# Kernel tuning notes

Measured on AMD Instinct MI355X. Metric: run time of the kernel, lower is better.

Reference implementation:

```python
import jax, jax.numpy as jnp
import numpy as np

LAMBD = 0.2   # model.lambd
T_MAX = 1000  # model.T
TOL = 1e-10


def _softshrink(v, lam):
    return jnp.sign(v) * jnp.maximum(jnp.abs(v) - lam, 0.0)


def setup_inputs() -> dict:
    key = jax.random.key(0)
    k1, k2, k3 = jax.random.split(key, 3)
    n, m, N = 64, 256, 1024
    D = jax.random.normal(k1, (n, m), dtype=jnp.float32)
    D = D / jnp.linalg.norm(D, axis=0)                      # unit-norm atoms
    w = jax.random.normal(k2, (m,), dtype=jnp.float32)
    w = w / jnp.linalg.norm(w)
    x = jax.random.normal(k3, (N, n), dtype=jnp.float32)
    x = x / jnp.linalg.norm(x, axis=1, keepdims=True)       # unit-norm samples (as in generate_data)
    return {"x": x, "D": D, "w": w}


def _encode(x_t, D, lambd):
    # x_t: (n, N), D: (n, m). Faithful to encode(): ISTA with detached D/x,
    # then per-sample least-squares refinement on the support (vectorized as
    # a masked batched solve instead of a python loop over samples).
    m = D.shape[1]
    Dg = jax.lax.stop_gradient(D)
    xg = jax.lax.stop_gradient(x_t)
    # eta = 1/||D||_2^2 is a constant in torch (computed from numpy at init)
    eta = jax.lax.stop_gradient(1.0 / jnp.linalg.norm(Dg, ord=2) ** 2)
    thr = lambd * eta

    z0 = _softshrink(eta * (Dg.T @ xg), thr)                # (m, N)

    def cond(c):
        i, _, diff = c
        return (i < T_MAX) & (diff >= TOL)

    def body(c):
        i, z, _ = c
        res = Dg @ z - xg                                   # (n, N)
        znew = _softshrink(z - eta * (Dg.T @ res), thr)     # (m, N)
        return (i + 1, znew, jnp.linalg.norm(znew - z))

    _, z, _ = jax.lax.while_loop(
        cond, body, (jnp.int32(0), z0, jnp.array(jnp.inf, dtype=x_t.dtype))
    )
    z = jax.lax.stop_gradient(z)                            # ISTA output is fully detached in torch

    # Support refinement: alfa[S,i] = inv(D_S^T D_S) (D_S^T x_i - lambd*signs_S)
    mask = z != 0                                           # (m, N) support sets
    signs = jnp.sign(z)                                     # constant (sign has zero grad)
    M = mask.T.astype(x_t.dtype)                            # (N, m)
    G = D.T @ D                                             # (m, m) Gram (with grad, model.D)
    b = M * (x_t.T @ D - lambd * signs.T)                   # (N, m), zero off-support
    # Masked Gram: identity on off-support rows/cols -> block solve equals submatrix solve
    A = M[:, :, None] * M[:, None, :] * G[None] \
        + jnp.eye(m, dtype=x_t.dtype) * (1.0 - M)[:, :, None]   # (N, m, m)
    solved = jnp.linalg.solve(A, b[..., None])[..., 0]      # (N, m)
    alfa = jnp.where(mask, solved.T, z)                     # (m, N)
    return alfa


def reference(x, D, w):
    # x: (N, n). forward(): z = encode(x); y = w @ z; pred = [y, -y]
    z = _encode(x.T, D, LAMBD)                              # (m, N)
    y = w @ z                                               # (N,)
    return jnp.stack([y, -y], axis=1)                       # (N, 2)
```

## Files before the change

### kernel.cpp

```cpp
#include <hip/hip_runtime.h>

#define LAMBD 0.2f
#define KMAX 128
#define KS 64

using half8 = __attribute__((ext_vector_type(8))) _Float16;
using f32x4 = __attribute__((ext_vector_type(4))) float;

__device__ __forceinline__ float sshrink(float v, float thr) {
    float c = fminf(fmaxf(v, -thr), thr);
    return v - c;
}

__device__ __forceinline__ unsigned pack2(_Float16 a, _Float16 b) {
    unsigned short ua = __builtin_bit_cast(unsigned short, a);
    unsigned short ub = __builtin_bit_cast(unsigned short, b);
    return (unsigned)ua | ((unsigned)ub << 16);
}

__global__ __launch_bounds__(256) void prep_all(const float* __restrict__ xg,
                                                const float* __restrict__ Dg,
                                                float* __restrict__ ws,
                                                float* __restrict__ Gfull,
                                                float* __restrict__ cbuf)
{
    const int t = threadIdx.x;
    if (blockIdx.x == 0) {
        __shared__ __align__(16) float Dc[256 * 68];
        __shared__ __align__(16) float Bm[64 * 68];
        __shared__ float vv[64];
        __shared__ float part[4 * 64];
        __shared__ float lamsh;

        for (int i = 0; i < 64; ++i)
            Dc[t * 68 + i] = Dg[i * 256 + t];
        __syncthreads();

        const int ti = t >> 4, tj = t & 15;
        float acc[4][4];
        #pragma unroll
        for (int r = 0; r < 4; ++r)
            #pragma unroll
            for (int c = 0; c < 4; ++c) acc[r][c] = 0.f;
        for (int mm = 0; mm < 256; ++mm) {
            const float4 A = *(const float4*)&Dc[mm * 68 + 4 * ti];
            const float4 Bv = *(const float4*)&Dc[mm * 68 + 4 * tj];
            const float Ae[4] = {A.x, A.y, A.z, A.w};
            const float Be[4] = {Bv.x, Bv.y, Bv.z, Bv.w};
            #pragma unroll
            for (int r = 0; r < 4; ++r)
                #pragma unroll
                for (int c = 0; c < 4; ++c)
                    acc[r][c] += Ae[r] * Be[c];
        }
        #pragma unroll
        for (int r = 0; r < 4; ++r)
            #pragma unroll
            for (int c = 0; c < 4; ++c)
                Bm[(4 * ti + r) * 68 + (4 * tj + c)] = acc[r][c];
        if (t < 64) vv[t] = 0.125f;
        __syncthreads();

        for (int itp = 0; itp < 40; ++itp) {
            const int p = t >> 6, i = t & 63;
            float partial = 0.f;
            #pragma unroll
            for (int jj = 0; jj < 16; ++jj) {
                const int j = p * 16 + jj;
                partial += Bm[j * 68 + i] * vv[j];
            }
            part[p * 64 + i] = partial;
            __syncthreads();
            if (t < 64) {
                float nv = part[t] + part[64 + t] + part[128 + t] + part[192 + t];
                float n2 = nv * nv;
                for (int d = 1; d < 64; d <<= 1) n2 += __shfl_xor(n2, d);
                vv[t] = nv * rsqrtf(n2);
                if (t == 0) lamsh = n2;
            }
            __syncthreads();
        }
        if (t == 0) ws[0] = 1.0f / sqrtf(lamsh);
    } else {
        __shared__ float xsh[4][64];
        const int r = blockIdx.x - 1;
        const int s0 = r * 4;
        xsh[t >> 6][t & 63] = xg[s0 * 64 + t];
        __syncthreads();

        float accG = 0.f, a0 = 0.f, a1 = 0.f, a2 = 0.f, a3 = 0.f;
        #pragma unroll
        for (int i = 0; i < 64; ++i) {
            const float dv = Dg[i * 256 + t];
            const float dr = Dg[i * 256 + r];
            accG += dr * dv;
            a0 += xsh[0][i] * dv;
            a1 += xsh[1][i] * dv;
            a2 += xsh[2][i] * dv;
            a3 += xsh[3][i] * dv;
        }
        Gfull[r * 256 + t] = accG;
        cbuf[(s0 + 0) * 256 + t] = a0;
        cbuf[(s0 + 1) * 256 + t] = a1;
        cbuf[(s0 + 2) * 256 + t] = a2;
        cbuf[(s0 + 3) * 256 + t] = a3;
    }
}

__global__ __launch_bounds__(256, 1) void ista_solve(const float* __restrict__ cbuf,
                                                     const float* __restrict__ Gfull,
                                                     const float* __restrict__ ws,
                                                     const float* __restrict__ wg,
                                                     float* __restrict__ out)
{
    __shared__ __align__(16) _Float16 dbuf[2][16][264];
    __shared__ int chgs[4];
    __shared__ __align__(16) float znb[4][264];
    __shared__ __align__(16) float GmPool[16640];
    __shared__ int   idxPool[256];
    __shared__ float sgnPool[256];
    __shared__ float rhsF[KMAX];
    __shared__ float solF[KMAX];
    __shared__ int   big4[4];
    __shared__ int   kbig;

    const int t = threadIdx.x;
    const int w = t >> 6, l = t & 63;
    const int n = l & 15, kg = l >> 4;
    const int s0 = blockIdx.x * 4;
    const float s = ws[0];
    const float thr = LAMBD * s;
    const float S = 1.0f / 2048.0f;
    const float FLUSH = 6.2e-5f;

    half8 wh[4][8], wl[4][8];
    #pragma unroll
    for (int a = 0; a < 4; ++a) {
        const int row = 64 * w + 16 * a + n;
        #pragma unroll
        for (int kt = 0; kt < 8; ++kt) {
            const float4 g0 = *(const float4*)&Gfull[row * 256 + kt * 32 + kg * 8];
            const float4 g1 = *(const float4*)&Gfull[row * 256 + kt * 32 + kg * 8 + 4];
            const float ge[8] = {g0.x, g0.y, g0.z, g0.w, g1.x, g1.y, g1.z, g1.w};
            half8 h, lo;
            #pragma unroll
            for (int j = 0; j < 8; ++j) {
                const int col = kt * 32 + kg * 8 + j;
                const float wv = (row == col ? 1.0f : 0.0f) - s * ge[j];
                const _Float16 whj = (_Float16)wv;
                h[j] = whj;
                lo[j] = (_Float16)((wv - (float)whj) * 2048.0f);
            }
            wh[a][kt] = h;
            wl[a][kt] = lo;
        }
    }

    float bv[4][4], y[4][4], zo[4][4], zn[4][4];
    #pragma unroll
    for (int a = 0; a < 4; ++a)
        #pragma unroll
        for (int jj = 0; jj < 4; ++jj) {
            const int row = 64 * w + 16 * a + 4 * kg + jj;
            bv[a][jj] = (n < 4) ? s * cbuf[(s0 + n) * 256 + row] : 0.f;
            y[a][jj] = 0.f;
            zo[a][jj] = 0.f;
        }

    f32x4 acc1[4], acc2[4];
    #pragma unroll
    for (int a = 0; a < 4; ++a) {
        acc1[a] = (f32x4){0.f, 0.f, 0.f, 0.f};
        acc2[a] = (f32x4){0.f, 0.f, 0.f, 0.f};
    }

    float tk = 1.0f;
    int cur = 0;
    for (int it = 0; ; ++it) {
        const float tk1 = 0.5f * (1.0f + sqrtf(1.0f + 4.0f * tk * tk));
        const float beta = (tk - 1.0f) / tk1;
        bool anyflag = false;
        _Float16 dh16[4][4];
        #pragma unroll
        for (int a = 0; a < 4; ++a)
            #pragma unroll
            for (int jj = 0; jj < 4; ++jj) {
                const float P = acc1[a][jj] + S * acc2[a][jj];
                const float z = sshrink(P + bv[a][jj], thr);
                zn[a][jj] = z;
                const float yn = z + beta * (z - zo[a][jj]);
                zo[a][jj] = z;
                const float d = yn - y[a][jj];
                const bool live = fabsf(d) >= FLUSH;
                anyflag |= live;
                const _Float16 hd = live ? (_Float16)d : (_Float16)0.0f;
                dh16[a][jj] = hd;
                y[a][jj] += (float)hd;
            }
        tk = tk1;
        if (it == 1000) break;

        const int anyw = __any(anyflag);
        if (l == 0) chgs[w] = anyw;
        #pragma unroll
        for (int a = 0; a < 4; ++a) {
            const unsigned lo = pack2(dh16[a][0], dh16[a][1]);
            const unsigned hi = pack2(dh16[a][2], dh16[a][3]);
            *(uint2*)&dbuf[cur][n][64 * w + 16 * a + 4 * kg] = make_uint2(lo, hi);
        }
        __syncthreads();
        if (!(chgs[0] | chgs[1] | chgs[2] | chgs[3])) break;

        half8 dh[8];
        #pragma unroll
        for (int kt = 0; kt < 8; ++kt)
            dh[kt] = *(const half8*)&dbuf[cur][n][kt * 32 + kg * 8];

        #pragma unroll
        for (int kt = 0; kt < 8; ++kt)
            #pragma unroll
            for (int a = 0; a < 4; ++a) {
                acc1[a] = __builtin_amdgcn_mfma_f32_16x16x32_f16(wh[a][kt], dh[kt], acc1[a], 0, 0, 0);
                acc2[a] = __builtin_amdgcn_mfma_f32_16x16x32_f16(wl[a][kt], dh[kt], acc2[a], 0, 0, 0);
            }
        cur ^= 1;
    }

    if (n < 4) {
        #pragma unroll
        for (int a = 0; a < 4; ++a) {
            float4 v = make_float4(zn[a][0], zn[a][1], zn[a][2], zn[a][3]);
            *(float4*)&znb[n][64 * w + 16 * a + 4 * kg] = v;
        }
    }
    __syncthreads();

    const int sample = s0 + w;
    float* Gw = GmPool + w * (KS * (KS + 1));
    int*   idxW = idxPool + w * KS;
    float* sgnW = sgnPool + w * KS;

    const float4 zz = *(const float4*)&znb[w][4 * l];
    const int c0 = zz.x != 0.f, c1 = zz.y != 0.f, c2 = zz.z != 0.f, c3 = zz.w != 0.f;
    const int cnt = c0 + c1 + c2 + c3;
    int scan = cnt;
    for (int d = 1; d < 64; d <<= 1) {
        const int v = __shfl_up(scan, d);
        if (l >= d) scan += v;
    }
    int o = scan - cnt;
    const int k = __shfl(scan, 63);
    if (l == 0) big4[w] = (k > KS) ? 1 : 0;

    if (k == 0) {
        if (l == 0) { out[sample * 2] = 0.f; out[sample * 2 + 1] = 0.f; }
    } else if (k <= KS) {
        if (c0) { idxW[o] = 4 * l + 0; sgnW[o] = zz.x > 0.f ? 1.f : -1.f; ++o; }
        if (c1) { idxW[o] = 4 * l + 1; sgnW[o] = zz.y > 0.f ? 1.f : -1.f; ++o; }
        if (c2) { idxW[o] = 4 * l + 2; sgnW[o] = zz.z > 0.f ? 1.f : -1.f; ++o; }
        if (c3) { idxW[o] = 4 * l + 3; sgnW[o] = zz.w > 0.f ? 1.f : -1.f; ++o; }
        __builtin_amdgcn_wave_barrier();

        const int   ib = idxW[(l < k) ? l : (k - 1)];
        const float sg = (l < k) ? sgnW[l] : 0.f;
        float rhs = (l < k) ? (cbuf[sample * 256 + ib] - LAMBD * sg) : 0.f;

        for (int a = 0; a < k; ++a) {
            const int ra = __shfl(ib, a);
            if (l < k) Gw[a * (KS + 1) + l] = Gfull[ra * 256 + ib];
        }
        __builtin_amdgcn_wave_barrier();

        float dinv = 0.f;
        for (int j = 0; j < k; ++j) {
            const float Gjj = Gw[j * (KS + 1) + j];
            const float Ljj = sqrtf(fmaxf(Gjj, 1e-30f));
            const float iv = 1.0f / Ljj;
            float Laj = 0.f;
            if (l == j) { Gw[j * (KS + 1) + j] = Ljj; dinv = iv; }
            if (l > j && l < k) { Laj = Gw[l * (KS + 1) + j] * iv; Gw[l * (KS + 1) + j] = Laj; }
            __builtin_amdgcn_wave_barrier();
            for (int b = j + 1; b < k; ++b) {
                const float Lbj = Gw[b * (KS + 1) + j];
                if (l >= b && l < k) Gw[l * (KS + 1) + b] -= Laj * Lbj;
            }
            __builtin_amdgcn_wave_barrier();
        }

        float yv = rhs;
        for (int j = 0; j < k; ++j) {
            const float Laj = Gw[l * (KS + 1) + j];
            const float yjf = __shfl(yv, j) * __shfl(dinv, j);
            if (l == j) yv = yjf;
            if (l > j) yv -= Laj * yjf;
        }
        float xv = yv;
        for (int j = k - 1; j >= 0; --j) {
            const float Lja = Gw[j * (KS + 1) + l];
            const float xjf = __shfl(xv, j) * __shfl(dinv, j);
            if (l == j) xv = xjf;
            if (l < j) xv -= Lja * xjf;
        }

        float acc = (l < k) ? wg[ib] * xv : 0.f;
        for (int d = 1; d < 64; d <<= 1) acc += __shfl_xor(acc, d);
        if (l == 0) { out[sample * 2] = acc; out[sample * 2 + 1] = -acc; }
    }
    __syncthreads();

    for (int sw = 0; sw < 4; ++sw) {
        if (!big4[sw]) continue;
        const int smp = s0 + sw;
        if (w == 0) {
            const float4 z2 = *(const float4*)&znb[sw][4 * l];
            const int d0 = z2.x != 0.f, d1 = z2.y != 0.f, d2 = z2.z != 0.f, d3 = z2.w != 0.f;
            const int cn = d0 + d1 + d2 + d3;
            int sc = cn;
            for (int d = 1; d < 64; d <<= 1) {
                const int v = __shfl_up(sc, d);
                if (l >= d) sc += v;
            }
            int oo = sc - cn;
            int kk = __shfl(sc, 63);
            if (kk > KMAX) kk = KMAX;
            if (l == 0) kbig = kk;
            if (d0) { if (oo < KMAX) { idxPool[oo] = 4 * l + 0; sgnPool[oo] = z2.x > 0.f ? 1.f : -1.f; } ++oo; }
            if (d1) { if (oo < KMAX) { idxPool[oo] = 4 * l + 1; sgnPool[oo] = z2.y > 0.f ? 1.f : -1.f; } ++oo; }
            if (d2) { if (oo < KMAX) { idxPool[oo] = 4 * l + 2; sgnPool[oo] = z2.z > 0.f ? 1.f : -1.f; } ++oo; }
            if (d3) { if (oo < KMAX) { idxPool[oo] = 4 * l + 3; sgnPool[oo] = z2.w > 0.f ? 1.f : -1.f; } ++oo; }
        }
        __syncthreads();
        const int kk = kbig;
        float* Gb = GmPool;

        for (int a = 0; a < kk; ++a) {
            const int ra = idxPool[a];
            for (int b = t; b < kk; b += 256)
                Gb[a * (KMAX + 1) + b] = Gfull[ra * 256 + idxPool[b]];
        }
        for (int a = t; a < kk; a += 256)
            rhsF[a] = cbuf[smp * 256 + idxPool[a]] - LAMBD * sgnPool[a];
        __syncthreads();

        for (int j = 0; j < kk; ++j) {
            const float Ljj = sqrtf(fmaxf(Gb[j * (KMAX + 1) + j], 1e-30f));
            const float inv = 1.0f / Ljj;
            if (t == 0) Gb[j * (KMAX + 1) + j] = Ljj;
            for (int a = j + 1 + t; a < kk; a += 256)
                Gb[a * (KMAX + 1) + j] *= inv;
            __syncthreads();
            for (int b = j + 1; b < kk; ++b) {
                const float Lbj = Gb[b * (KMAX + 1) + j];
                const int a = b + t;
                if (a < kk) Gb[a * (KMAX + 1) + b] -= Gb[a * (KMAX + 1) + j] * Lbj;
            }
            __syncthreads();
        }
        for (int j = 0; j < kk; ++j) {
            const float yj = rhsF[j] / Gb[j * (KMAX + 1) + j];
            if (t == 0) solF[j] = yj;
            for (int a = j + 1 + t; a < kk; a += 256)
                rhsF[a] -= Gb[a * (KMAX + 1) + j] * yj;
            __syncthreads();
        }
        for (int j = kk - 1; j >= 0; --j) {
            const float xj = solF[j] / Gb[j * (KMAX + 1) + j];
            if (t == 0) solF[j] = xj;
            for (int a = t; a < j; a += 256)
                solF[a] -= Gb[j * (KMAX + 1) + a] * xj;
            __syncthreads();
        }
        float acc = 0.f;
        for (int a = t; a < kk; a += 256)
            acc += wg[idxPool[a]] * solF[a];
        for (int d = 1; d < 64; d <<= 1) acc += __shfl_xor(acc, d);
        if (l == 0) atomicAdd(&solF[0], 0.f);
        if (l == 0) rhsF[64 + w] = acc;
        __syncthreads();
        if (t == 0) {
            const float tot = rhsF[64] + rhsF[65] + rhsF[66] + rhsF[67];
            out[smp * 2] = tot;
            out[smp * 2 + 1] = -tot;
        }
        __syncthreads();
    }
}

extern "C" void kernel_launch(void* const* d_in, const int* in_sizes, int n_in,
                              void* d_out, int out_size, void* d_ws, size_t ws_size,
                              hipStream_t stream) {
    const float* x = (const float*)d_in[0];
    const float* D = (const float*)d_in[1];
    const float* w = (const float*)d_in[2];
    float* out = (float*)d_out;
    float* ws  = (float*)d_ws;

    float* Gfull = ws + 256;
    float* cbuf  = ws + 256 + 65536;

    prep_all<<<257, 256, 0, stream>>>(x, D, ws, Gfull, cbuf);
    ista_solve<<<256, 256, 0, stream>>>(cbuf, Gfull, ws, w, out);
}
```

Before: 237.5 us.

## Use hi-only MFMA in early ISTA phase, add lo correction after sign support stabilizes

```diff
diff --git a/kernel.cpp b/kernel.cpp
--- a/kernel.cpp
+++ b/kernel.cpp
@@ -3,6 +3,8 @@
 #define LAMBD 0.2f
 #define KMAX 128
 #define KS 64
+#define SSA 16
+#define ACAP 600
 
 using half8 = __attribute__((ext_vector_type(8))) _Float16;
 using f32x4 = __attribute__((ext_vector_type(4))) float;
@@ -114,6 +116,7 @@
                                                      float* __restrict__ out)
 {
     __shared__ __align__(16) _Float16 dbuf[2][16][264];
+    __shared__ __align__(16) _Float16 ybuf[16][264];
     __shared__ int chgs[4];
     __shared__ __align__(16) float znb[4][264];
     __shared__ __align__(16) float GmPool[16640];
@@ -175,11 +178,12 @@
     }
 
     float tk = 1.0f;
-    int cur = 0;
+    int cur = 0, stable = 0;
+    bool phase2 = false;
     for (int it = 0; ; ++it) {
         const float tk1 = 0.5f * (1.0f + sqrtf(1.0f + 4.0f * tk * tk));
         const float beta = (tk - 1.0f) / tk1;
-        bool anyflag = false;
+        bool anychg = false, anylive = false;
         _Float16 dh16[4][4];
         #pragma unroll
         for (int a = 0; a < 4; ++a)
@@ -187,12 +191,14 @@
             for (int jj = 0; jj < 4; ++jj) {
                 const float P = acc1[a][jj] + S * acc2[a][jj];
                 const float z = sshrink(P + bv[a][jj], thr);
+                const float zp = zo[a][jj];
+                anychg |= ((z > 0.f) != (zp > 0.f)) | ((z < 0.f) != (zp < 0.f));
                 zn[a][jj] = z;
-                const float yn = z + beta * (z - zo[a][jj]);
+                const float yn = z + beta * (z - zp);
                 zo[a][jj] = z;
                 const float d = yn - y[a][jj];
                 const bool live = fabsf(d) >= FLUSH;
-                anyflag |= live;
+                anylive |= live;
                 const _Float16 hd = live ? (_Float16)d : (_Float16)0.0f;
                 dh16[a][jj] = hd;
                 y[a][jj] += (float)hd;
@@ -200,7 +206,8 @@
         tk = tk1;
         if (it == 1000) break;
 
-        const int anyw = __any(anyflag);
+        const bool flag = phase2 ? anylive : anychg;
+        const int anyw = __any(flag);
         if (l == 0) chgs[w] = anyw;
         #pragma unroll
         for (int a = 0; a < 4; ++a) {
@@ -209,7 +216,31 @@
             *(uint2*)&dbuf[cur][n][64 * w + 16 * a + 4 * kg] = make_uint2(lo, hi);
         }
         __syncthreads();
-        if (!(chgs[0] | chgs[1] | chgs[2] | chgs[3])) break;
+        const int anyblk = chgs[0] | chgs[1] | chgs[2] | chgs[3];
+        if (phase2 && !anyblk) break;
+        stable = anyblk ? 0 : stable + 1;
+
+        const bool do_trans = (!phase2) && (stable >= SSA || it >= ACAP);
+        if (do_trans) {
+            #pragma unroll
+            for (int a = 0; a < 4; ++a) {
+                const unsigned lo = pack2((_Float16)y[a][0], (_Float16)y[a][1]);
+                const unsigned hi = pack2((_Float16)y[a][2], (_Float16)y[a][3]);
+                *(uint2*)&ybuf[n][64 * w + 16 * a + 4 * kg] = make_uint2(lo, hi);
+            }
+            __syncthreads();
+            half8 yh[8];
+            #pragma unroll
+            for (int kt = 0; kt < 8; ++kt)
+                yh[kt] = *(const half8*)&ybuf[n][kt * 32 + kg * 8];
+            #pragma unroll
+            for (int kt = 0; kt < 8; ++kt)
+                #pragma unroll
+                for (int a = 0; a < 4; ++a)
+                    acc2[a] = __builtin_amdgcn_mfma_f32_16x16x32_f16(wl[a][kt], yh[kt], acc2[a], 0, 0, 0);
+            phase2 = true;
+            stable = 0;
+        }
 
         half8 dh[8];
         #pragma unroll
@@ -219,10 +250,15 @@
         #pragma unroll
         for (int kt = 0; kt < 8; ++kt)
             #pragma unroll
-            for (int a = 0; a < 4; ++a) {
+            for (int a = 0; a < 4; ++a)
                 acc1[a] = __builtin_amdgcn_mfma_f32_16x16x32_f16(wh[a][kt], dh[kt], acc1[a], 0, 0, 0);
-                acc2[a] = __builtin_amdgcn_mfma_f32_16x16x32_f16(wl[a][kt], dh[kt], acc2[a], 0, 0, 0);
-            }
+        if (phase2 && !do_trans) {
+            #pragma unroll
+            for (int kt = 0; kt < 8; ++kt)
+                #pragma unroll
+                for (int a = 0; a < 4; ++a)
+                    acc2[a] = __builtin_amdgcn_mfma_f32_16x16x32_f16(wl[a][kt], dh[kt], acc2[a], 0, 0, 0);
+        }
         cur ^= 1;
     }
 
@@ -374,7 +410,6 @@
         for (int a = t; a < kk; a += 256)
             acc += wg[idxPool[a]] * solF[a];
         for (int d = 1; d < 64; d <<= 1) acc += __shfl_xor(acc, d);
-        if (l == 0) atomicAdd(&solF[0], 0.f);
         if (l == 0) rhsF[64 + w] = acc;
         __syncthreads();
         if (t == 0) {
```

After: 262.2 us. 10.4% more time.
